# Kernel tuning notes

Measured on AMD Instinct MI355X. Metric: run time of the kernel, lower is better.

The kernel has to match this reference:

```python
import jax, jax.numpy as jnp
import numpy as np

B, C, H, W, N = 4, 5, 256, 256, 2048
HW = H * W


def setup_inputs() -> dict:
    key = jax.random.key(0)
    ks = jax.random.split(key, 8)
    s = 1.0 / np.sqrt(C)
    x = jax.random.normal(ks[0], (B, C, H, W), jnp.float32)
    Wq = jax.random.normal(ks[1], (C, C), jnp.float32) * s
    Wk = jax.random.normal(ks[2], (C, C), jnp.float32) * s
    Wv = jax.random.normal(ks[3], (C, C), jnp.float32) * s
    bq = jnp.zeros((C,), jnp.float32)
    bk = jnp.zeros((C,), jnp.float32)
    bv = jnp.zeros((C,), jnp.float32)
    gamma = jnp.zeros((1,), jnp.float32)  # nn.Parameter(torch.zeros(1))
    idx_b = jax.random.randint(ks[4], (N,), 0, B, jnp.int32)
    idx_h = jax.random.randint(ks[5], (N,), 0, H, jnp.int32)
    idx_w = jax.random.randint(ks[6], (N,), 0, W, jnp.int32)
    return {"x": x, "Wq": Wq, "bq": bq, "Wk": Wk, "bk": bk, "Wv": Wv,
            "bv": bv, "gamma": gamma, "idx_b": idx_b, "idx_h": idx_h, "idx_w": idx_w}


def _conv1x1(x, Wt, b):
    # 1x1 conv == per-pixel channel mix
    return jnp.einsum('oc,bchw->bohw', Wt, x) + b[None, :, None, None]


def reference(x, Wq, bq, Wk, bk, Wv, bv, gamma, idx_b, idx_h, idx_w):
    q = _conv1x1(x, Wq, bq)
    k = _conv1x1(x, Wk, bk)
    v = _conv1x1(x, Wv, bv)
    q_pix = q[idx_b, :, idx_h, idx_w]              # [N, C] gathered query pixels
    Kf = k.reshape(B, C, HW)
    Vf = v.reshape(B, C, HW)
    # energy[n, l] = sum_c q_pix[n, c] * Kf[idx_b[n], c, l]
    # channel loop (C=5, fixed) avoids materializing [N, C, HW]
    energy = jnp.zeros((N, HW), x.dtype)
    for c in range(C):
        energy = energy + q_pix[:, c:c + 1] * Kf[idx_b, c]   # [N, HW]
    attn = jax.nn.softmax(energy, axis=-1)                   # [N, HW]
    out = jnp.stack([jnp.sum(Vf[idx_b, c] * attn, axis=-1) for c in range(C)],
                    axis=1)                                  # [N, C]
    upd = (gamma[0] + 0.1) * out + x[idx_b, :, idx_h, idx_w]
    # y starts as a detached copy of x; selected pixels are overwritten
    y = jax.lax.stop_gradient(x).at[idx_b, :, idx_h, idx_w].set(upd)
    return y
```

## Files before the change

kernel.cpp:

```cpp
#include <hip/hip_runtime.h>


constexpr int HWC = 256 * 256;
constexpr int Bc  = 4;
constexpr int Nq  = 2048;
constexpr int Wc  = 256;

constexpr int TPB   = 40;
constexpr int SPLIT = 16;

constexpr float LOG2E = 1.4426950408889634f;
constexpr float BIAS2 = -14.0f * LOG2E;

constexpr size_t K8_BYTES  = (size_t)Bc * HWC * 8 * 2;
constexpr size_t VT_BYTES  = (size_t)Bc * 5 * HWC * 2;
constexpr size_t QP_BYTES  = (size_t)Nq * 8 * 2;
constexpr size_t PART_BYTES = (size_t)SPLIT * Nq * 6 * 4;
constexpr size_t K8_OFF   = 0;
constexpr size_t VT_OFF   = K8_OFF + K8_BYTES;
constexpr size_t QP16_OFF = VT_OFF + VT_BYTES;
constexpr size_t PART_OFF = QP16_OFF + QP_BYTES;
constexpr size_t PERM_OFF = PART_OFF + PART_BYTES;
constexpr size_t CNT_OFF  = PERM_OFF + (size_t)Bc * Nq * 4;

typedef __attribute__((ext_vector_type(8))) _Float16 f16x8;
typedef __attribute__((ext_vector_type(4))) float f32x4;
union FU { uint4 u; f16x8 h; };

#if defined(__has_builtin)
#if __has_builtin(__builtin_amdgcn_exp2f)
#define EXP2F(x) __builtin_amdgcn_exp2f(x)
#endif
#endif
#ifndef EXP2F
#define EXP2F(x) exp2f(x)
#endif

__device__ inline unsigned pack2(float a, float b) {
  typedef __attribute__((ext_vector_type(2))) __fp16 fp16x2;
  union { fp16x2 h; unsigned u; } r;
  r.h = __builtin_amdgcn_cvt_pkrtz(a, b);
  return r.u;
}

__global__ __launch_bounds__(256) void k1_prep(
    const float* __restrict__ x,
    const float* __restrict__ Wq, const float* __restrict__ bq,
    const float* __restrict__ Wk, const float* __restrict__ bk,
    const float* __restrict__ Wv, const float* __restrict__ bv,
    const int* __restrict__ idx_b, const int* __restrict__ idx_h,
    const int* __restrict__ idx_w,
    float* __restrict__ y, char* __restrict__ wsb) {
  const int tid = threadIdx.x;
  _Float16* K8   = (_Float16*)(wsb + K8_OFF);
  _Float16* VT   = (_Float16*)(wsb + VT_OFF);
  _Float16* QP16 = (_Float16*)(wsb + QP16_OFF);
  if (blockIdx.x >= 1024) {
    if (blockIdx.x == 1032) {
      __shared__ int lcnt[Bc];
      if (tid < Bc) lcnt[tid] = 0;
      __syncthreads();
      int* perm = (int*)(wsb + PERM_OFF);
#pragma unroll
      for (int qi = 0; qi < 8; ++qi) {
        const int n = qi * 256 + tid;
        const int b = idx_b[n];
        const int pos = atomicAdd(&lcnt[b], 1);
        perm[b * Nq + pos] = n;
      }
      __syncthreads();
      if (tid < Bc) ((int*)(wsb + CNT_OFF))[tid] = lcnt[tid];
      return;
    }
    const int n = (blockIdx.x - 1024) * 256 + tid;
    const int b = idx_b[n];
    const int s = idx_h[n] * Wc + idx_w[n];
    float xv[5];
#pragma unroll
    for (int c = 0; c < 5; ++c) xv[c] = x[(size_t)(b * 5 + c) * HWC + s];
    float q[5];
#pragma unroll
    for (int o = 0; o < 5; ++o) {
      float t = bq[o];
#pragma unroll
      for (int c = 0; c < 5; ++c) t = fmaf(Wq[o * 5 + c], xv[c], t);
      q[o] = t * LOG2E;
    }
    uint4 row;
    row.x = pack2(q[0], q[1]);
    row.y = pack2(q[2], q[3]);
    row.z = pack2(q[4], 0.f);
    row.w = 0u;
    *(uint4*)(QP16 + (size_t)n * 8) = row;
    return;
  }
  const int gid = blockIdx.x * 256 + tid;
  const int b   = gid >> 16;
  const int s   = gid & (HWC - 1);
  float xv[5];
#pragma unroll
  for (int c = 0; c < 5; ++c) {
    const size_t off = (size_t)(b * 5 + c) * HWC + s;
    xv[c] = x[off];
    y[off] = xv[c];
  }
  float kk[5], vv[5];
#pragma unroll
  for (int o = 0; o < 5; ++o) {
    kk[o] = bk[o];
    vv[o] = bv[o];
#pragma unroll
    for (int c = 0; c < 5; ++c) {
      kk[o] = fmaf(Wk[o * 5 + c], xv[c], kk[o]);
      vv[o] = fmaf(Wv[o * 5 + c], xv[c], vv[o]);
    }
  }
  uint4 krow;
  krow.x = pack2(kk[0], kk[1]);
  krow.y = pack2(kk[2], kk[3]);
  krow.z = pack2(kk[4], 0.f);
  krow.w = 0u;
  *(uint4*)(K8 + (size_t)(b * HWC + s) * 8) = krow;
#pragma unroll
  for (int c = 0; c < 5; ++c)
    VT[(size_t)(b * 5 + c) * HWC + s] = (_Float16)vv[c];
}

__global__ __launch_bounds__(256) void k2_attn(char* __restrict__ wsb) {
  const int chunk = blockIdx.x;
  const int tile  = blockIdx.y;
  const int bb    = tile / TPB;
  const int tt    = tile % TPB;
  const int cb    = ((const int*)(wsb + CNT_OFF))[bb];
  const int j0    = tt * 16;
  if (j0 >= cb) return;
  const int* perm = (const int*)(wsb + PERM_OFF) + bb * Nq;

  const int tid  = threadIdx.x;
  const int wv   = tid >> 6;
  const int lane = tid & 63;
  const int quad = lane >> 4;
  const int l15  = lane & 15;

  __shared__ _Float16 Pbuf[4][16][64];
  __shared__ float    Ored[4][16][6];

  const _Float16* K8b  = (const _Float16*)(wsb + K8_OFF) + (size_t)bb * HWC * 8;
  const _Float16* Vtb  = (const _Float16*)(wsb + VT_OFF) + (size_t)bb * 5 * HWC;
  const _Float16* QP16 = (const _Float16*)(wsb + QP16_OFF);

  _Float16* Pw = &Pbuf[wv][0][0];
  const int swzg = 2 * (l15 & 7);
  const int rowb = l15 << 6;
  const int woff0 = rowb + (((0 * 4 + quad) ^ swzg) << 2);
  const int woff1 = rowb + (((1 * 4 + quad) ^ swzg) << 2);
  const int woff2 = rowb + (((2 * 4 + quad) ^ swzg) << 2);
  const int woff3 = rowb + (((3 * 4 + quad) ^ swzg) << 2);
  const int roff0 = rowb + (((0 + 2 * quad) ^ swzg) << 2);
  const int roff1 = rowb + (((8 + 2 * quad) ^ swzg) << 2);

  FU qf; qf.u = make_uint4(0u, 0u, 0u, 0u);
  {
    const int jq = j0 + l15;
    if (quad == 0) {
      const int n = (jq < cb) ? perm[jq] : 0;
      qf.u = *(const uint4*)(QP16 + (size_t)n * 8);
    }
  }
  FU vf0, vf1;
  {
    const unsigned ones = (l15 == 5) ? 0x3C003C00u : 0u;
    vf0.u = make_uint4(ones, ones, ones, ones);
    vf1.u = vf0.u;
  }
  FU kf0, kf1, kf2, kf3;
  kf0.u = make_uint4(0u, 0u, 0u, 0u);
  kf1.u = kf0.u; kf2.u = kf0.u; kf3.u = kf0.u;

  const f32x4 bias = {BIAS2, BIAS2, BIAS2, BIAS2};
  f32x4 oacc = {0.f, 0.f, 0.f, 0.f};

  const _Float16* vplane = Vtb + (size_t)l15 * HWC;

  int s0 = chunk * (HWC / SPLIT) + wv * (HWC / SPLIT / 4);
  for (int it = 0; it < HWC / SPLIT / 4 / 64; ++it, s0 += 64) {
    if (quad == 0) {
      kf0.u = *(const uint4*)(K8b + (size_t)(s0 +  0 + l15) * 8);
      kf1.u = *(const uint4*)(K8b + (size_t)(s0 + 16 + l15) * 8);
      kf2.u = *(const uint4*)(K8b + (size_t)(s0 + 32 + l15) * 8);
      kf3.u = *(const uint4*)(K8b + (size_t)(s0 + 48 + l15) * 8);
    }
    if (l15 < 5) {
      vf0.u = *(const uint4*)(vplane + s0 +  0 + 8 * quad);
      vf1.u = *(const uint4*)(vplane + s0 + 32 + 8 * quad);
    }
    f32x4 e0 = __builtin_amdgcn_mfma_f32_16x16x32_f16(kf0.h, qf.h, bias, 0, 0, 0);
    f32x4 e1 = __builtin_amdgcn_mfma_f32_16x16x32_f16(kf1.h, qf.h, bias, 0, 0, 0);
    f32x4 e2 = __builtin_amdgcn_mfma_f32_16x16x32_f16(kf2.h, qf.h, bias, 0, 0, 0);
    f32x4 e3 = __builtin_amdgcn_mfma_f32_16x16x32_f16(kf3.h, qf.h, bias, 0, 0, 0);
    uint2 w0, w1, w2, w3;
    w0.x = pack2(EXP2F(e0.x), EXP2F(e0.y)); w0.y = pack2(EXP2F(e0.z), EXP2F(e0.w));
    w1.x = pack2(EXP2F(e1.x), EXP2F(e1.y)); w1.y = pack2(EXP2F(e1.z), EXP2F(e1.w));
    w2.x = pack2(EXP2F(e2.x), EXP2F(e2.y)); w2.y = pack2(EXP2F(e2.z), EXP2F(e2.w));
    w3.x = pack2(EXP2F(e3.x), EXP2F(e3.y)); w3.y = pack2(EXP2F(e3.z), EXP2F(e3.w));
    *(uint2*)(Pw + woff0) = w0;
    *(uint2*)(Pw + woff1) = w1;
    *(uint2*)(Pw + woff2) = w2;
    *(uint2*)(Pw + woff3) = w3;
    FU pa0, pa1;
    pa0.h = *(const f16x8*)(Pw + roff0);
    pa1.h = *(const f16x8*)(Pw + roff1);
    oacc = __builtin_amdgcn_mfma_f32_16x16x32_f16(pa0.h, vf0.h, oacc, 0, 0, 0);
    oacc = __builtin_amdgcn_mfma_f32_16x16x32_f16(pa1.h, vf1.h, oacc, 0, 0, 0);
  }

  if (l15 < 6) {
    Ored[wv][4 * quad + 0][l15] = oacc.x;
    Ored[wv][4 * quad + 1][l15] = oacc.y;
    Ored[wv][4 * quad + 2][l15] = oacc.z;
    Ored[wv][4 * quad + 3][l15] = oacc.w;
  }
  __syncthreads();
  if (tid < 96) {
    const int q = tid / 6, comp = tid % 6;
    const float s = Ored[0][q][comp] + Ored[1][q][comp] +
                    Ored[2][q][comp] + Ored[3][q][comp];
    const int j = j0 + q;
    if (j < cb) {
      const int n = perm[j];
      ((float*)(wsb + PART_OFF))[((size_t)chunk * Nq + n) * 6 + comp] = s;
    }
  }
}

__global__ __launch_bounds__(256) void k3_final(
    const float* __restrict__ x, const float* __restrict__ gamma,
    const int* __restrict__ idx_b, const int* __restrict__ idx_h,
    const int* __restrict__ idx_w, float* __restrict__ y,
    const char* __restrict__ wsb) {
  const int n = blockIdx.x * 256 + threadIdx.x;
  const float* part = (const float*)(wsb + PART_OFF);
  float l = 0.f, o[5] = {0.f, 0.f, 0.f, 0.f, 0.f};
#pragma unroll
  for (int ch = 0; ch < SPLIT; ++ch) {
    const float* p = part + ((size_t)ch * Nq + n) * 6;
#pragma unroll
    for (int c = 0; c < 5; ++c) o[c] += p[c];
    l += p[5];
  }
  const float gsc = gamma[0] + 0.1f;
  const float inv = 1.0f / l;
  const int b = idx_b[n], h = idx_h[n], w = idx_w[n];
  const int s = h * Wc + w;
#pragma unroll
  for (int c = 0; c < 5; ++c) {
    const size_t off = (size_t)(b * 5 + c) * HWC + s;
    y[off] = fmaf(gsc, o[c] * inv, x[off]);
  }
}

extern "C" void kernel_launch(void* const* d_in, const int* in_sizes, int n_in,
                              void* d_out, int out_size, void* d_ws, size_t ws_size,
                              hipStream_t stream) {
  const float* x     = (const float*)d_in[0];
  const float* Wq    = (const float*)d_in[1];
  const float* bq    = (const float*)d_in[2];
  const float* Wk    = (const float*)d_in[3];
  const float* bk    = (const float*)d_in[4];
  const float* Wv    = (const float*)d_in[5];
  const float* bv    = (const float*)d_in[6];
  const float* gamma = (const float*)d_in[7];
  const int* idx_b   = (const int*)d_in[8];
  const int* idx_h   = (const int*)d_in[9];
  const int* idx_w   = (const int*)d_in[10];
  float* y  = (float*)d_out;
  char* wsb = (char*)d_ws;

  k1_prep<<<1033, 256, 0, stream>>>(x, Wq, bq, Wk, bk, Wv, bv,
                                    idx_b, idx_h, idx_w, y, wsb);
  k2_attn<<<dim3(SPLIT, Bc * TPB), 256, 0, stream>>>(wsb);
  k3_final<<<Nq / 256, 256, 0, stream>>>(x, gamma, idx_b, idx_h, idx_w, y, wsb);
}
```

Baseline: 119.5 us.

## Software-pipeline attention loop with double-buffered K/V registers and P buffer

```diff
diff --git a/kernel.cpp b/kernel.cpp
--- a/kernel.cpp
+++ b/kernel.cpp
@@ -126,7 +126,44 @@
     VT[(size_t)(b * 5 + c) * HWC + s] = (_Float16)vv[c];
 }
 
-__global__ __launch_bounds__(256) void k2_attn(char* __restrict__ wsb) {
+#define BODY(KC0, KC1, KC2, KC3, KN0, KN1, KN2, KN3, VN0, VN1,                \
+             NBASE, DOPV, DOLOAD, RPW, WPW)                                   \
+  do {                                                                        \
+    f32x4 e0 = __builtin_amdgcn_mfma_f32_16x16x32_f16(KC0.h, qf.h, bias, 0, 0, 0); \
+    f32x4 e1 = __builtin_amdgcn_mfma_f32_16x16x32_f16(KC1.h, qf.h, bias, 0, 0, 0); \
+    f32x4 e2 = __builtin_amdgcn_mfma_f32_16x16x32_f16(KC2.h, qf.h, bias, 0, 0, 0); \
+    f32x4 e3 = __builtin_amdgcn_mfma_f32_16x16x32_f16(KC3.h, qf.h, bias, 0, 0, 0); \
+    if (DOPV) {                                                               \
+      FU pa0, pa1;                                                            \
+      pa0.h = *(const f16x8*)((RPW) + roff0);                                 \
+      pa1.h = *(const f16x8*)((RPW) + roff1);                                 \
+      oacc = __builtin_amdgcn_mfma_f32_16x16x32_f16(pa0.h, VN0.h, oacc, 0, 0, 0); \
+      oacc = __builtin_amdgcn_mfma_f32_16x16x32_f16(pa1.h, VN1.h, oacc, 0, 0, 0); \
+    }                                                                         \
+    if (DOLOAD) {                                                             \
+      if (quad == 0) {                                                        \
+        KN0.u = *(const uint4*)(K8b + (size_t)((NBASE) +  0 + l15) * 8);      \
+        KN1.u = *(const uint4*)(K8b + (size_t)((NBASE) + 16 + l15) * 8);      \
+        KN2.u = *(const uint4*)(K8b + (size_t)((NBASE) + 32 + l15) * 8);      \
+        KN3.u = *(const uint4*)(K8b + (size_t)((NBASE) + 48 + l15) * 8);      \
+      }                                                                       \
+      if (l15 < 5) {                                                          \
+        VN0.u = *(const uint4*)(vplane + (NBASE) +  0 + 8 * quad);            \
+        VN1.u = *(const uint4*)(vplane + (NBASE) + 32 + 8 * quad);            \
+      }                                                                       \
+    }                                                                         \
+    uint2 w0, w1, w2, w3;                                                     \
+    w0.x = pack2(EXP2F(e0.x), EXP2F(e0.y)); w0.y = pack2(EXP2F(e0.z), EXP2F(e0.w)); \
+    w1.x = pack2(EXP2F(e1.x), EXP2F(e1.y)); w1.y = pack2(EXP2F(e1.z), EXP2F(e1.w)); \
+    w2.x = pack2(EXP2F(e2.x), EXP2F(e2.y)); w2.y = pack2(EXP2F(e2.z), EXP2F(e2.w)); \
+    w3.x = pack2(EXP2F(e3.x), EXP2F(e3.y)); w3.y = pack2(EXP2F(e3.z), EXP2F(e3.w)); \
+    *(uint2*)((WPW) + woff0) = w0;                                            \
+    *(uint2*)((WPW) + woff1) = w1;                                            \
+    *(uint2*)((WPW) + woff2) = w2;                                            \
+    *(uint2*)((WPW) + woff3) = w3;                                            \
+  } while (0)
+
+__global__ __launch_bounds__(256, 4) void k2_attn(char* __restrict__ wsb) {
   const int chunk = blockIdx.x;
   const int tile  = blockIdx.y;
   const int bb    = tile / TPB;
@@ -142,14 +179,15 @@
   const int quad = lane >> 4;
   const int l15  = lane & 15;
 
-  __shared__ _Float16 Pbuf[4][16][64];
+  __shared__ _Float16 Pbuf[4][2][16][64];
   __shared__ float    Ored[4][16][6];
 
   const _Float16* K8b  = (const _Float16*)(wsb + K8_OFF) + (size_t)bb * HWC * 8;
   const _Float16* Vtb  = (const _Float16*)(wsb + VT_OFF) + (size_t)bb * 5 * HWC;
   const _Float16* QP16 = (const _Float16*)(wsb + QP16_OFF);
 
-  _Float16* Pw = &Pbuf[wv][0][0];
+  _Float16* PwE = &Pbuf[wv][0][0][0];
+  _Float16* PwO = &Pbuf[wv][1][0][0];
   const int swzg = 2 * (l15 & 7);
   const int rowb = l15 << 6;
   const int woff0 = rowb + (((0 * 4 + quad) ^ swzg) << 2);
@@ -167,51 +205,57 @@
       qf.u = *(const uint4*)(QP16 + (size_t)n * 8);
     }
   }
-  FU vf0, vf1;
+  FU vA0, vA1, vB0, vB1;
   {
     const unsigned ones = (l15 == 5) ? 0x3C003C00u : 0u;
-    vf0.u = make_uint4(ones, ones, ones, ones);
-    vf1.u = vf0.u;
-  }
-  FU kf0, kf1, kf2, kf3;
-  kf0.u = make_uint4(0u, 0u, 0u, 0u);
-  kf1.u = kf0.u; kf2.u = kf0.u; kf3.u = kf0.u;
+    vA0.u = make_uint4(ones, ones, ones, ones);
+    vA1.u = vA0.u; vB0.u = vA0.u; vB1.u = vA0.u;
+  }
+  FU kA0, kA1, kA2, kA3, kB0, kB1, kB2, kB3;
+  kA0.u = make_uint4(0u, 0u, 0u, 0u);
+  kA1.u = kA0.u; kA2.u = kA0.u; kA3.u = kA0.u;
+  kB0.u = kA0.u; kB1.u = kA0.u; kB2.u = kA0.u; kB3.u = kA0.u;
 
   const f32x4 bias = {BIAS2, BIAS2, BIAS2, BIAS2};
   f32x4 oacc = {0.f, 0.f, 0.f, 0.f};
 
   const _Float16* vplane = Vtb + (size_t)l15 * HWC;
 
-  int s0 = chunk * (HWC / SPLIT) + wv * (HWC / SPLIT / 4);
-  for (int it = 0; it < HWC / SPLIT / 4 / 64; ++it, s0 += 64) {
-    if (quad == 0) {
-      kf0.u = *(const uint4*)(K8b + (size_t)(s0 +  0 + l15) * 8);
-      kf1.u = *(const uint4*)(K8b + (size_t)(s0 + 16 + l15) * 8);
-      kf2.u = *(const uint4*)(K8b + (size_t)(s0 + 32 + l15) * 8);
-      kf3.u = *(const uint4*)(K8b + (size_t)(s0 + 48 + l15) * 8);
-    }
-    if (l15 < 5) {
-      vf0.u = *(const uint4*)(vplane + s0 +  0 + 8 * quad);
-      vf1.u = *(const uint4*)(vplane + s0 + 32 + 8 * quad);
-    }
-    f32x4 e0 = __builtin_amdgcn_mfma_f32_16x16x32_f16(kf0.h, qf.h, bias, 0, 0, 0);
-    f32x4 e1 = __builtin_amdgcn_mfma_f32_16x16x32_f16(kf1.h, qf.h, bias, 0, 0, 0);
-    f32x4 e2 = __builtin_amdgcn_mfma_f32_16x16x32_f16(kf2.h, qf.h, bias, 0, 0, 0);
-    f32x4 e3 = __builtin_amdgcn_mfma_f32_16x16x32_f16(kf3.h, qf.h, bias, 0, 0, 0);
-    uint2 w0, w1, w2, w3;
-    w0.x = pack2(EXP2F(e0.x), EXP2F(e0.y)); w0.y = pack2(EXP2F(e0.z), EXP2F(e0.w));
-    w1.x = pack2(EXP2F(e1.x), EXP2F(e1.y)); w1.y = pack2(EXP2F(e1.z), EXP2F(e1.w));
-    w2.x = pack2(EXP2F(e2.x), EXP2F(e2.y)); w2.y = pack2(EXP2F(e2.z), EXP2F(e2.w));
-    w3.x = pack2(EXP2F(e3.x), EXP2F(e3.y)); w3.y = pack2(EXP2F(e3.z), EXP2F(e3.w));
-    *(uint2*)(Pw + woff0) = w0;
-    *(uint2*)(Pw + woff1) = w1;
-    *(uint2*)(Pw + woff2) = w2;
-    *(uint2*)(Pw + woff3) = w3;
+  const int s0 = chunk * (HWC / SPLIT) + wv * (HWC / SPLIT / 4);
+
+  if (quad == 0) {
+    kA0.u = *(const uint4*)(K8b + (size_t)(s0 +  0 + l15) * 8);
+    kA1.u = *(const uint4*)(K8b + (size_t)(s0 + 16 + l15) * 8);
+    kA2.u = *(const uint4*)(K8b + (size_t)(s0 + 32 + l15) * 8);
+    kA3.u = *(const uint4*)(K8b + (size_t)(s0 + 48 + l15) * 8);
+  }
+  if (l15 < 5) {
+    vA0.u = *(const uint4*)(vplane + s0 +  0);
+    vA1.u = *(const uint4*)(vplane + s0 + 32);
+  }
+  if (l15 < 5 && quad != 0) {
+    vA0.u = *(const uint4*)(vplane + s0 +  0 + 8 * quad);
+    vA1.u = *(const uint4*)(vplane + s0 + 32 + 8 * quad);
+  }
+
+  BODY(kA0, kA1, kA2, kA3, kB0, kB1, kB2, kB3, vB0, vB1,
+       s0 + 64, false, true, PwE, PwE);
+#pragma unroll
+  for (int p = 0; p < 7; ++p) {
+    const int it = 1 + 2 * p;
+    BODY(kB0, kB1, kB2, kB3, kA0, kA1, kA2, kA3, vA0, vA1,
+         s0 + 64 * (it + 1), true, true, PwE, PwO);
+    BODY(kA0, kA1, kA2, kA3, kB0, kB1, kB2, kB3, vB0, vB1,
+         s0 + 64 * (it + 2), true, true, PwO, PwE);
+  }
+  BODY(kB0, kB1, kB2, kB3, kA0, kA1, kA2, kA3, vA0, vA1,
+       0, true, false, PwE, PwO);
+  {
     FU pa0, pa1;
-    pa0.h = *(const f16x8*)(Pw + roff0);
-    pa1.h = *(const f16x8*)(Pw + roff1);
-    oacc = __builtin_amdgcn_mfma_f32_16x16x32_f16(pa0.h, vf0.h, oacc, 0, 0, 0);
-    oacc = __builtin_amdgcn_mfma_f32_16x16x32_f16(pa1.h, vf1.h, oacc, 0, 0, 0);
+    pa0.h = *(const f16x8*)(PwO + roff0);
+    pa1.h = *(const f16x8*)(PwO + roff1);
+    oacc = __builtin_amdgcn_mfma_f32_16x16x32_f16(pa0.h, vB0.h, oacc, 0, 0, 0);
+    oacc = __builtin_amdgcn_mfma_f32_16x16x32_f16(pa1.h, vB1.h, oacc, 0, 0, 0);
   }
 
   if (l15 < 6) {
```

New measurement: 118.6 us. Within noise of the previous version (-0.7%).
